# Kernel optimization log

Measured on AMD Instinct MI355X. Metric: run time of the kernel, lower is better.

## Reference

```python
import jax, jax.numpy as jnp
import numpy as np

TOPK = 8
EPS = 1e-12  # F.normalize eps


def setup_inputs() -> dict:
    key = jax.random.key(0)
    k1, k2 = jax.random.split(key)
    feats = jax.random.normal(k1, (4, 256, 64, 64), dtype=jnp.float32)
    logits = jax.random.normal(k2, (4, 1, 64, 64), dtype=jnp.float32)
    return {"feats": feats, "logits": logits}


def reference(feats, logits):
    b, c, h, w = feats.shape
    n = h * w
    feat_flat = feats.reshape(b, c, n)
    # F.normalize(dim=1): x / max(||x||_2, eps)
    norm = jnp.sqrt(jnp.sum(feat_flat * feat_flat, axis=1, keepdims=True))
    feat_norm = feat_flat / jnp.maximum(norm, EPS)
    # sim[b,i,j] = <f_i, f_j>  -> [B, N, N]
    sim = jnp.einsum('bci,bcj->bij', feat_norm, feat_norm)
    k = min(TOPK, n)
    _, idx = jax.lax.top_k(sim, k)  # [B, N, k] indices
    prob = jax.nn.sigmoid(logits).reshape(b, n)  # [B, N]
    # gathered[b,i,j] = prob[b, idx[b,i,j]]
    gathered = jax.vmap(lambda p, i: p[i])(prob, idx)  # [B, N, k]
    anchor = prob[:, :, None]  # [B, N, 1] broadcast over k
    loss = jnp.mean(jnp.abs(anchor - gathered))
    return loss
```

## Files before the change

### kernel.cpp

```cpp
#include <hip/hip_runtime.h>
#include <hip/hip_bf16.h>

typedef _Float16 half8 __attribute__((ext_vector_type(8)));
typedef unsigned short ushort8 __attribute__((ext_vector_type(8)));
typedef float floatx4 __attribute__((ext_vector_type(4)));

#define B_ 4
#define C_ 256
#define N_ 4096
#define NT 32
#define TRI 528

#define OFF_FN    ((size_t)0)
#define OFF_PROB  ((size_t)(8u << 20))
#define OFF_PART  (OFF_PROB + 65536)
#define OFF_TOP   ((size_t)(16u << 20))

__device__ __forceinline__ void gl_lds16(const void* g, void* l) {
    __builtin_amdgcn_global_load_lds(
        (const __attribute__((address_space(1))) void*)g,
        (__attribute__((address_space(3))) void*)l,
        16, 0, 0);
}

__device__ __forceinline__ void cas(uint32_t& a, uint32_t& b) {
    uint32_t hi = max(a, b); b = min(a, b); a = hi;
}

__device__ __forceinline__ void sort8(uint32_t v[8]) {
    cas(v[0],v[1]); cas(v[2],v[3]); cas(v[4],v[5]); cas(v[6],v[7]);
    cas(v[0],v[2]); cas(v[1],v[3]); cas(v[4],v[6]); cas(v[5],v[7]);
    cas(v[1],v[2]); cas(v[5],v[6]);
    cas(v[0],v[4]); cas(v[1],v[5]); cas(v[2],v[6]); cas(v[3],v[7]);
    cas(v[2],v[4]); cas(v[3],v[5]);
    cas(v[1],v[2]); cas(v[3],v[4]); cas(v[5],v[6]);
}

__device__ __forceinline__ void merge8(uint32_t r[8], const uint32_t n[8]) {
    uint32_t m[8];
#pragma unroll
    for (int i = 0; i < 8; ++i) m[i] = max(r[i], n[7 - i]);
    cas(m[0],m[4]); cas(m[1],m[5]); cas(m[2],m[6]); cas(m[3],m[7]);
    cas(m[0],m[2]); cas(m[1],m[3]); cas(m[4],m[6]); cas(m[5],m[7]);
    cas(m[0],m[1]); cas(m[2],m[3]); cas(m[4],m[5]); cas(m[6],m[7]);
#pragma unroll
    for (int i = 0; i < 8; ++i) r[i] = m[i];
}

#define TS 68
__global__ __launch_bounds__(256) void prep_kernel(const float* __restrict__ feats,
                                                   const float* __restrict__ logits,
                                                   _Float16* __restrict__ fn,
                                                   float* __restrict__ prob) {
    __shared__ __align__(16) float T[C_ * TS];
    __shared__ float S[256];
    __shared__ float I[64];

    const int t  = threadIdx.x;
    const int b  = blockIdx.x >> 6;
    const int i0 = (blockIdx.x & 63) * 64;
    const float* fb = feats + (size_t)b * C_ * N_;

#pragma unroll
    for (int k = 0; k < 16; ++k) {
        int ch = t + k * 256;
        int row = ch >> 4, col4 = ch & 15;
        float4 v = *(const float4*)(fb + (size_t)row * N_ + i0 + col4 * 4);
        *(float4*)&T[row * TS + col4 * 4] = v;
    }
    __syncthreads();
    {
        int i = t & 63, cq = t >> 6;
        float ss = 0.f;
#pragma unroll 8
        for (int j = 0; j < 64; ++j) { float v = T[(cq * 64 + j) * TS + i]; ss += v * v; }
        S[cq * 64 + i] = ss;
    }
    __syncthreads();
    if (t < 64) {
        float ss = S[t] + S[64 + t] + S[128 + t] + S[192 + t];
        I[t] = 1.f / fmaxf(sqrtf(ss), 1e-12f);
        float lg = logits[b * N_ + i0 + t];
        prob[b * N_ + i0 + t] = 1.f / (1.f + expf(-lg));
    }
    __syncthreads();
    {
        int i = t >> 2, chunk = t & 3;
        float s = I[i];
        _Float16* fr = fn + ((size_t)(b * N_ + i0 + i)) * C_ + chunk * 64;
#pragma unroll
        for (int v8 = 0; v8 < 8; ++v8) {
            half8 h;
#pragma unroll
            for (int e = 0; e < 8; ++e)
                h[e] = (_Float16)(T[(chunk * 64 + v8 * 8 + e) * TS + i] * s);
            *(half8*)(fr + v8 * 8) = h;
        }
    }
}

#define CSH 136
__global__ __launch_bounds__(256, 4) void gram_sel_kernel(const _Float16* __restrict__ fn,
                                                          uint32_t* __restrict__ top) {
    __shared__ __align__(16) char smem[128 * CSH * 2];
    _Float16* As = (_Float16*)smem;
    _Float16* Bs = (_Float16*)(smem + 16384);
    unsigned short* Ch = (unsigned short*)smem;
    uint32_t* Ms = (uint32_t*)smem;

    const int t    = threadIdx.x;
    const int lane = t & 63;
    const int w    = t >> 6;
    const int m16  = lane & 15;
    const int q    = lane >> 4;
    const int wm   = w & 1;
    const int wn   = w >> 1;

    const int bid0 = blockIdx.x;
    const int bid  = (bid0 & 7) * 264 + (bid0 >> 3);

    const int b = bid / TRI;
    const int u = bid - b * TRI;
    int it = (int)(32.5f - sqrtf(32.5f * 32.5f - 2.0f * (float)u));
    while (u >= (it + 1) * (65 - (it + 1)) / 2) ++it;
    while (u < it * (65 - it) / 2) --it;
    const int jt = it + (u - it * (65 - it) / 2);
    const bool diag = (it == jt);

    const int i0 = it * 128, j0 = jt * 128;
    const _Float16* fnb = fn + (size_t)b * N_ * C_;

    const int srowb = t >> 3;
    const int schunk = (t & 7) ^ (srowb & 7);
    const int sw = m16 & 7;

    floatx4 acc[4][4];
#pragma unroll
    for (int mi = 0; mi < 4; ++mi)
#pragma unroll
        for (int ni = 0; ni < 4; ++ni) acc[mi][ni] = floatx4{0.f, 0.f, 0.f, 0.f};

    for (int kc = 0; kc < 4; ++kc) {
#pragma unroll
        for (int r = 0; r < 4; ++r) {
            int row = r * 32 + srowb;
            const _Float16* gA = fnb + (size_t)(i0 + row) * C_ + kc * 64 + schunk * 8;
            const _Float16* gB = fnb + (size_t)(j0 + row) * C_ + kc * 64 + schunk * 8;
            gl_lds16(gA, (char*)As + r * 4096 + t * 16);
            gl_lds16(gB, (char*)Bs + r * 4096 + t * 16);
        }
        __syncthreads();
#pragma unroll
        for (int kk = 0; kk < 2; ++kk) {
            const int ko = ((kk * 4 + q) ^ sw) * 8;
            half8 af[4], bf[4];
#pragma unroll
            for (int mi = 0; mi < 4; ++mi)
                af[mi] = *(const half8*)&As[(wm * 64 + mi * 16 + m16) * 64 + ko];
#pragma unroll
            for (int ni = 0; ni < 4; ++ni)
                bf[ni] = *(const half8*)&Bs[(wn * 64 + ni * 16 + m16) * 64 + ko];
#pragma unroll
            for (int mi = 0; mi < 4; ++mi)
#pragma unroll
                for (int ni = 0; ni < 4; ++ni)
                    acc[mi][ni] = __builtin_amdgcn_mfma_f32_16x16x32_f16(af[mi], bf[ni], acc[mi][ni], 0, 0, 0);
        }
        __syncthreads();
    }

#pragma unroll
    for (int ni = 0; ni < 4; ++ni)
#pragma unroll
        for (int mi = 0; mi < 4; ++mi) {
            const int col = wn * 64 + ni * 16 + m16;
            const int row = wm * 64 + mi * 16 + q * 4;
#pragma unroll
            for (int p = 0; p < 2; ++p) {
                auto pk2 = __builtin_amdgcn_cvt_pkrtz(acc[mi][ni][2 * p], acc[mi][ni][2 * p + 1]);
                uint32_t bits = __builtin_bit_cast(uint32_t, pk2);
                uint32_t s = (bits >> 15) & 0x00010001u;
                uint32_t fl = bits ^ (s * 0x7FFFu + 0x80008000u);
                *(uint32_t*)&Ch[col * CSH + row + 2 * p] = fl;
            }
        }
    __syncthreads();

    uint32_t cpk[8], rpk[8];
    {
        const int ccol = t >> 1, cr0 = (t & 1) * 64;
        const unsigned short* cc = &Ch[ccol * CSH + cr0];
        const int ibase = i0 + cr0;
#pragma unroll
        for (int g = 0; g < 8; ++g) {
            ushort8 v = *(const ushort8*)(cc + g * 8);
            uint32_t cand[8];
#pragma unroll
            for (int e = 0; e < 8; ++e)
                cand[e] = ((uint32_t)v[e] << 16) | (uint32_t)(ibase + g * 8 + e);
            sort8(cand);
            if (g == 0) {
#pragma unroll
                for (int s = 0; s < 8; ++s) cpk[s] = cand[s];
            } else merge8(cpk, cand);
        }
    }
    if (!diag) {
        const int rrow = t >> 1, ch0 = (t & 1) * 64;
        const unsigned short* cr = &Ch[ch0 * CSH + rrow];
        const int jbase = j0 + ch0;
#pragma unroll
        for (int g = 0; g < 8; ++g) {
            uint32_t cand[8];
#pragma unroll
            for (int e = 0; e < 8; ++e)
                cand[e] = ((uint32_t)cr[(g * 8 + e) * CSH] << 16) | (uint32_t)(jbase + g * 8 + e);
            sort8(cand);
            if (g == 0) {
#pragma unroll
                for (int s = 0; s < 8; ++s) rpk[s] = cand[s];
            } else merge8(rpk, cand);
        }
    }
    __syncthreads();

    if (t & 1) {
#pragma unroll
        for (int s = 0; s < 8; ++s) Ms[(t >> 1) * 8 + s] = cpk[s];
        if (!diag) {
#pragma unroll
            for (int s = 0; s < 8; ++s) Ms[1024 + (t >> 1) * 8 + s] = rpk[s];
        }
    }
    __syncthreads();
    if (!(t & 1)) {
        uint32_t o[8];
#pragma unroll
        for (int s = 0; s < 8; ++s) o[s] = Ms[(t >> 1) * 8 + s];
        merge8(cpk, o);
        uint32_t* dst = top + (((size_t)b * N_ + j0 + (t >> 1)) * 32 + it) * 8;
        *(uint4*)dst       = make_uint4(cpk[0], cpk[1], cpk[2], cpk[3]);
        *(uint4*)(dst + 4) = make_uint4(cpk[4], cpk[5], cpk[6], cpk[7]);
        if (!diag) {
#pragma unroll
            for (int s = 0; s < 8; ++s) o[s] = Ms[1024 + (t >> 1) * 8 + s];
            merge8(rpk, o);
            uint32_t* dst2 = top + (((size_t)b * N_ + i0 + (t >> 1)) * 32 + jt) * 8;
            *(uint4*)dst2       = make_uint4(rpk[0], rpk[1], rpk[2], rpk[3]);
            *(uint4*)(dst2 + 4) = make_uint4(rpk[4], rpk[5], rpk[6], rpk[7]);
        }
    }
}

__global__ __launch_bounds__(256) void merge_kernel(const uint32_t* __restrict__ top,
                                                    const float* __restrict__ prob,
                                                    float* __restrict__ partials) {
    __shared__ float red[4];
    const int t = threadIdx.x;
    const int lane = t & 63;
    const int w = t >> 6;
    const int rg = blockIdx.x * 4 + w;
    const int b = rg >> 12;

    uint4 v4 = ((const uint4*)(top + (size_t)rg * 256))[lane];
    uint32_t v[4] = {v4.x, v4.y, v4.z, v4.w};
    uint32_t m = max(max(v[0], v[1]), max(v[2], v[3]));

    const float* pb = prob + (b << 12);
    float p_r = prob[rg];
    float contrib = 0.f;
#pragma unroll
    for (int k = 0; k < 8; ++k) {
        uint32_t M = m;
#pragma unroll
        for (int off = 32; off; off >>= 1) M = max(M, (uint32_t)__shfl_xor((int)M, off));
        if (lane == k) contrib = fabsf(p_r - pb[M & 0xFFFu]);
#pragma unroll
        for (int s = 0; s < 4; ++s) v[s] = (v[s] == M) ? 0u : v[s];
        m = max(max(v[0], v[1]), max(v[2], v[3]));
    }
#pragma unroll
    for (int off = 32; off; off >>= 1) contrib += __shfl_xor(contrib, off);
    if (lane == 0) red[w] = contrib;
    __syncthreads();
    if (t == 0) partials[blockIdx.x] = red[0] + red[1] + red[2] + red[3];
}

__global__ __launch_bounds__(256) void final_kernel(const float* __restrict__ partials,
                                                    float* __restrict__ out) {
    __shared__ float red[256];
    int t = threadIdx.x;
    float s = 0.f;
#pragma unroll
    for (int k = 0; k < 16; ++k) s += partials[k * 256 + t];
    red[t] = s;
    __syncthreads();
    for (int off = 128; off > 0; off >>= 1) {
        if (t < off) red[t] += red[t + off];
        __syncthreads();
    }
    if (t == 0) out[0] = red[0] * (1.f / (B_ * N_ * 8.0f));
}

extern "C" void kernel_launch(void* const* d_in, const int* in_sizes, int n_in,
                              void* d_out, int out_size, void* d_ws, size_t ws_size,
                              hipStream_t stream) {
    const float* feats  = (const float*)d_in[0];
    const float* logits = (const float*)d_in[1];
    float* out = (float*)d_out;
    char* ws = (char*)d_ws;
    _Float16* fn   = (_Float16*)(ws + OFF_FN);
    float* prob    = (float*)(ws + OFF_PROB);
    float* parts   = (float*)(ws + OFF_PART);
    uint32_t* top  = (uint32_t*)(ws + OFF_TOP);

    prep_kernel<<<256, 256, 0, stream>>>(feats, logits, fn, prob);
    gram_sel_kernel<<<B_ * TRI, 256, 0, stream>>>(fn, top);
    merge_kernel<<<4096, 256, 0, stream>>>(top, prob, parts);
    final_kernel<<<1, 256, 0, stream>>>(parts, out);
}
```

Measured before the change: 124.8 us.

## Double-buffer Gram GEMM K-loop with async LDS loads and finer stages

Replaces the single-buffered K loop (four 64-wide chunks, each followed by a full sync) with a double-buffered pipeline of eight 32-wide chunks. The next stage's global-to-LDS loads are issued before computing on the current buffer, using explicit vmcnt waits and raw s_barrier calls wrapped in sched_barrier. The LDS layout changes to pack two rows per 128-byte line with an XOR swizzle. The epilogue also merges two 32-bit LDS stores into one 64-bit store. The aim is to hide global load latency behind MFMA work, at the cost of more barriers and hand-written waitcnt logic that could introduce ordering bugs.

```diff
diff --git a/kernel.cpp b/kernel.cpp
--- a/kernel.cpp
+++ b/kernel.cpp
@@ -21,6 +21,12 @@
         (const __attribute__((address_space(1))) void*)g,
         (__attribute__((address_space(3))) void*)l,
         16, 0, 0);
+}
+
+__device__ __forceinline__ void pipe_barrier() {
+    __builtin_amdgcn_sched_barrier(0);
+    __builtin_amdgcn_s_barrier();
+    __builtin_amdgcn_sched_barrier(0);
 }
 
 __device__ __forceinline__ void cas(uint32_t& a, uint32_t& b) {
@@ -103,8 +109,6 @@
 __global__ __launch_bounds__(256, 4) void gram_sel_kernel(const _Float16* __restrict__ fn,
                                                           uint32_t* __restrict__ top) {
     __shared__ __align__(16) char smem[128 * CSH * 2];
-    _Float16* As = (_Float16*)smem;
-    _Float16* Bs = (_Float16*)(smem + 16384);
     unsigned short* Ch = (unsigned short*)smem;
     uint32_t* Ms = (uint32_t*)smem;
 
@@ -130,43 +134,67 @@
     const int i0 = it * 128, j0 = jt * 128;
     const _Float16* fnb = fn + (size_t)b * N_ * C_;
 
-    const int srowb = t >> 3;
-    const int schunk = (t & 7) ^ (srowb & 7);
-    const int sw = m16 & 7;
-
     floatx4 acc[4][4];
 #pragma unroll
     for (int mi = 0; mi < 4; ++mi)
 #pragma unroll
         for (int ni = 0; ni < 4; ++ni) acc[mi][ni] = floatx4{0.f, 0.f, 0.f, 0.f};
 
-    for (int kc = 0; kc < 4; ++kc) {
-#pragma unroll
-        for (int r = 0; r < 4; ++r) {
-            int row = r * 32 + srowb;
-            const _Float16* gA = fnb + (size_t)(i0 + row) * C_ + kc * 64 + schunk * 8;
-            const _Float16* gB = fnb + (size_t)(j0 + row) * C_ + kc * 64 + schunk * 8;
-            gl_lds16(gA, (char*)As + r * 4096 + t * 16);
-            gl_lds16(gB, (char*)Bs + r * 4096 + t * 16);
-        }
-        __syncthreads();
-#pragma unroll
-        for (int kk = 0; kk < 2; ++kk) {
-            const int ko = ((kk * 4 + q) ^ sw) * 8;
-            half8 af[4], bf[4];
-#pragma unroll
-            for (int mi = 0; mi < 4; ++mi)
-                af[mi] = *(const half8*)&As[(wm * 64 + mi * 16 + m16) * 64 + ko];
+    auto stage = [&](int kc8, int bsel) {
+        char* base = smem + bsel * 16384;
+#pragma unroll
+        for (int r = 0; r < 2; ++r) {
+            const int L  = (t >> 3) + r * 32;
+            const int sl = (t & 7) ^ (L & 7);
+            const int row = 2 * L + (sl >> 2);
+            const int c   = sl & 3;
+            const _Float16* gA = fnb + (size_t)(i0 + row) * C_ + kc8 * 32 + c * 8;
+            const _Float16* gB = fnb + (size_t)(j0 + row) * C_ + kc8 * 32 + c * 8;
+            gl_lds16(gA, base + r * 4096 + t * 16);
+            gl_lds16(gB, base + 8192 + r * 4096 + t * 16);
+        }
+    };
+    auto compute = [&](int bsel) {
+        const char* Asb = smem + bsel * 16384;
+        const char* Bsb = Asb + 8192;
+        half8 af[4], bf[4];
+#pragma unroll
+        for (int mi = 0; mi < 4; ++mi) {
+            const int row = wm * 64 + mi * 16 + m16;
+            const int R = row >> 1;
+            const int slot = (((row & 1) << 2) | q) ^ (R & 7);
+            af[mi] = *(const half8*)(Asb + R * 128 + slot * 16);
+        }
+#pragma unroll
+        for (int ni = 0; ni < 4; ++ni) {
+            const int row = wn * 64 + ni * 16 + m16;
+            const int R = row >> 1;
+            const int slot = (((row & 1) << 2) | q) ^ (R & 7);
+            bf[ni] = *(const half8*)(Bsb + R * 128 + slot * 16);
+        }
+#pragma unroll
+        for (int mi = 0; mi < 4; ++mi)
 #pragma unroll
             for (int ni = 0; ni < 4; ++ni)
-                bf[ni] = *(const half8*)&Bs[(wn * 64 + ni * 16 + m16) * 64 + ko];
-#pragma unroll
-            for (int mi = 0; mi < 4; ++mi)
-#pragma unroll
-                for (int ni = 0; ni < 4; ++ni)
-                    acc[mi][ni] = __builtin_amdgcn_mfma_f32_16x16x32_f16(af[mi], bf[ni], acc[mi][ni], 0, 0, 0);
-        }
-        __syncthreads();
+                acc[mi][ni] = __builtin_amdgcn_mfma_f32_16x16x32_f16(af[mi], bf[ni], acc[mi][ni], 0, 0, 0);
+    };
+
+    stage(0, 0);
+    stage(1, 1);
+    asm volatile("s_waitcnt vmcnt(4)" ::: "memory");
+    pipe_barrier();
+#pragma unroll
+    for (int s = 0; s < 8; ++s) {
+        compute(s & 1);
+        pipe_barrier();
+        if (s < 6) {
+            stage(s + 2, s & 1);
+            asm volatile("s_waitcnt vmcnt(4)" ::: "memory");
+            pipe_barrier();
+        } else if (s == 6) {
+            asm volatile("s_waitcnt vmcnt(0)" ::: "memory");
+            pipe_barrier();
+        }
     }
 
 #pragma unroll
@@ -175,14 +203,15 @@
         for (int mi = 0; mi < 4; ++mi) {
             const int col = wn * 64 + ni * 16 + m16;
             const int row = wm * 64 + mi * 16 + q * 4;
+            uint32_t fl[2];
 #pragma unroll
             for (int p = 0; p < 2; ++p) {
                 auto pk2 = __builtin_amdgcn_cvt_pkrtz(acc[mi][ni][2 * p], acc[mi][ni][2 * p + 1]);
                 uint32_t bits = __builtin_bit_cast(uint32_t, pk2);
                 uint32_t s = (bits >> 15) & 0x00010001u;
-                uint32_t fl = bits ^ (s * 0x7FFFu + 0x80008000u);
-                *(uint32_t*)&Ch[col * CSH + row + 2 * p] = fl;
+                fl[p] = bits ^ (s * 0x7FFFu + 0x80008000u);
             }
+            *(uint2*)&Ch[col * CSH + row] = make_uint2(fl[0], fl[1]);
         }
     __syncthreads();
 
```

Result: no change. 122.9 us (-1.5%).
